# Performance work log

Hardware: AMD Instinct MI355X
Metric: run time of the kernel (lower is better)

The kernel has to match this reference:

```python
import jax, jax.numpy as jnp
import numpy as np

N = 50000          # nodes
E = 1250000        # edges (avg degree 25)
EMBED = 64
HIDS = [64, 64, 64]
EDGE_DIM = 7       # 1 + 6
VOCAB = 5 ** 8     # 390625
NEG_SLOPE = 0.01   # F.leaky_relu default


def setup_inputs() -> dict:
    key = jax.random.key(0)
    ks = jax.random.split(key, 14)
    L = len(HIDS)
    x = jax.random.randint(ks[0], (N,), 0, VOCAB)
    edge_index = jax.random.randint(ks[1], (2, E), 0, N)
    edge_attr = jax.random.normal(ks[2], (E, EDGE_DIM), dtype=jnp.float32)
    emb = jax.random.normal(ks[3], (VOCAB, EMBED), dtype=jnp.float32) * 0.02
    # all layers have in = out = 64, so params are stacked along layer axis
    lin1_w = jax.random.normal(ks[4], (L, EMBED + EDGE_DIM, HIDS[0]), dtype=jnp.float32) * 0.1
    att_l = jax.random.normal(ks[5], (L, HIDS[0]), dtype=jnp.float32) * 0.1
    att_r = jax.random.normal(ks[6], (L, EMBED), dtype=jnp.float32) * 0.1
    lin2_w = jax.random.normal(ks[7], (L, HIDS[0], HIDS[0]), dtype=jnp.float32) * 0.1
    gbias = jax.random.normal(ks[8], (L, HIDS[0]), dtype=jnp.float32) * 0.01
    d_cat = int(np.sum(HIDS)) + EMBED  # 256
    fc1_w = jax.random.normal(ks[9], (d_cat, 20), dtype=jnp.float32) * 0.05
    fc1_b = jax.random.normal(ks[10], (20,), dtype=jnp.float32) * 0.01
    fc2_w = jax.random.normal(ks[11], (20, 1), dtype=jnp.float32) * 0.1
    fc2_b = jax.random.normal(ks[12], (1,), dtype=jnp.float32) * 0.01
    return {"x": x, "edge_index": edge_index, "edge_attr": edge_attr, "emb": emb,
            "lin1_w": lin1_w, "att_l": att_l, "att_r": att_r, "lin2_w": lin2_w,
            "gbias": gbias, "fc1_w": fc1_w, "fc1_b": fc1_b, "fc2_w": fc2_w, "fc2_b": fc2_b}


def _gate_conv(h, src, dst, edge_attr, w1, al, ar, w2, b):
    # message from source j -> target i; attention softmax over edges sharing a target
    xj = jnp.concatenate([h[src], edge_attr], axis=-1)            # [E, in+7]
    xj = jax.nn.leaky_relu(xj @ w1, NEG_SLOPE)                    # [E, out]
    alpha = jax.nn.leaky_relu(jnp.sum(xj * al, -1) + jnp.sum(h[dst] * ar, -1), NEG_SLOPE)
    amax = jax.ops.segment_max(alpha, dst, num_segments=N)        # [N]
    ea = jnp.exp(alpha - amax[dst])                               # [E]
    denom = jax.ops.segment_sum(ea, dst, num_segments=N)          # [N]
    a = ea / (denom[dst] + 1e-16)
    msg = (xj @ w2) * a[:, None]                                  # [E, out]
    return jax.ops.segment_sum(msg, dst, num_segments=N) + b      # [N, out]


def reference(x, edge_index, edge_attr, emb, lin1_w, att_l, att_r, lin2_w,
              gbias, fc1_w, fc1_b, fc2_w, fc2_b):
    src, dst = edge_index[0], edge_index[1]
    h = emb[x]                                                    # [N, EMBED]
    feats = [h]
    for l in range(len(HIDS)):
        h = jax.nn.relu(_gate_conv(h, src, dst, edge_attr,
                                   lin1_w[l], att_l[l], att_r[l], lin2_w[l], gbias[l]))
        feats.append(h)
    hcat = jnp.concatenate(feats, axis=-1)                        # [N, 256]
    z = jax.nn.relu(hcat @ fc1_w + fc1_b)
    out = jax.nn.sigmoid(z @ fc2_w + fc2_b)
    return out.squeeze(-1)                                        # [N]
```

## Files before the change

### kernel.cpp

```cpp
#include <hip/hip_runtime.h>
#include <math.h>

#define NEG 0.01f

typedef _Float16 f16;
typedef f16 h2 __attribute__((ext_vector_type(2)));

__device__ __forceinline__ float lrelu(float x) { return x > 0.f ? x : NEG * x; }

__device__ __forceinline__ h2 lrelu2(h2 x) {
    h2 y = x * (f16)0.01f;
    return __builtin_elementwise_max(x, y);
}

__device__ __forceinline__ float q16_allsum(float v) {
    int x;
    x = __builtin_amdgcn_update_dpp(0, __float_as_int(v), 0xB1, 0xF, 0xF, true);  v += __int_as_float(x);
    x = __builtin_amdgcn_update_dpp(0, __float_as_int(v), 0x4E, 0xF, 0xF, true);  v += __int_as_float(x);
    x = __builtin_amdgcn_update_dpp(0, __float_as_int(v), 0x124, 0xF, 0xF, true); v += __int_as_float(x);
    x = __builtin_amdgcn_update_dpp(0, __float_as_int(v), 0x128, 0xF, 0xF, true); v += __int_as_float(x);
    return v;
}

__device__ __forceinline__ float x16_32_sum(float v) {
    v += __int_as_float(__builtin_amdgcn_ds_swizzle(__float_as_int(v), 0x401F));
    v += __shfl_xor(v, 32, 64);
    return v;
}

__global__ void k_zero(int* __restrict__ deg, int n,
                       const float* __restrict__ lin1, const float* __restrict__ attl,
                       uint4* __restrict__ wpack) {
    int i = blockIdx.x * blockDim.x + threadIdx.x;
    if (i < n) deg[i] = 0;
    if (i < 48) {
        int l = i >> 4, t = i & 15;
        const float* wb  = lin1 + (size_t)l * 71 * 64 + 64 * 64;
        const float* alp = attl + l * 64;
        unsigned int u[20];
#pragma unroll
        for (int j = 0; j < 4; j++) {
            int f = 4 * t + j;
            h2 a = { (f16)wb[f],       (f16)wb[64 + f]  }; u[j]      = __builtin_bit_cast(unsigned int, a);
            h2 b = { (f16)wb[128 + f], (f16)wb[192 + f] }; u[4 + j]  = __builtin_bit_cast(unsigned int, b);
            h2 c = { (f16)wb[256 + f], (f16)wb[320 + f] }; u[8 + j]  = __builtin_bit_cast(unsigned int, c);
            h2 d = { (f16)wb[384 + f], (f16)0.f         }; u[12 + j] = __builtin_bit_cast(unsigned int, d);
        }
        h2 e0 = { (f16)alp[4 * t],     (f16)alp[4 * t + 1] }; u[16] = __builtin_bit_cast(unsigned int, e0);
        h2 e1 = { (f16)alp[4 * t + 2], (f16)alp[4 * t + 3] }; u[17] = __builtin_bit_cast(unsigned int, e1);
        u[18] = 0; u[19] = 0;
        uint4* o = wpack + (size_t)i * 5;
        o[0] = make_uint4(u[0],  u[1],  u[2],  u[3]);
        o[1] = make_uint4(u[4],  u[5],  u[6],  u[7]);
        o[2] = make_uint4(u[8],  u[9],  u[10], u[11]);
        o[3] = make_uint4(u[12], u[13], u[14], u[15]);
        o[4] = make_uint4(u[16], u[17], u[18], u[19]);
    }
}

__global__ __launch_bounds__(256) void k_count_gemm(
    const int* __restrict__ dst, int* __restrict__ deg, int* __restrict__ rank,
    int E, int nbCnt,
    const int* __restrict__ x, const float* __restrict__ emb,
    const float* __restrict__ B, const float* __restrict__ ar,
    f16* __restrict__ g, float* __restrict__ r_out, int N)
{
    __shared__ __align__(16) float sA[64][68];
    __shared__ __align__(16) float sB[64 * 64];
    __shared__ float sar[64];
    if ((int)blockIdx.x < nbCnt) {
        int e = blockIdx.x * 256 + threadIdx.x;
        if (e < E) rank[e] = atomicAdd(&deg[dst[e]], 1);
        return;
    }
    int tid = threadIdx.x;
    int row0 = ((int)blockIdx.x - nbCnt) * 64;

    {
        const float4* b4 = (const float4*)B;
        float4* s4 = (float4*)sB;
        for (int i = tid; i < 1024; i += 256) s4[i] = b4[i];
    }
    if (tid < 64) sar[tid] = ar[tid];

#pragma unroll
    for (int pass = 0; pass < 4; ++pass) {
        int nl = pass * 16 + (tid & 15);
        int k4 = (tid >> 4) * 4;
        int n = row0 + nl; if (n >= N) n = N - 1;
        float4 v = *(const float4*)(emb + (size_t)x[n] * 64 + k4);
        sA[k4 + 0][nl] = v.x; sA[k4 + 1][nl] = v.y;
        sA[k4 + 2][nl] = v.z; sA[k4 + 3][nl] = v.w;
    }
    __syncthreads();

    int tr = tid >> 4, tc = tid & 15;
    int r0 = tr * 4, c0 = tc * 4;
    float acc[4][4];
#pragma unroll
    for (int i = 0; i < 4; i++)
#pragma unroll
        for (int j = 0; j < 4; j++) acc[i][j] = 0.f;

#pragma unroll 4
    for (int k = 0; k < 64; ++k) {
        float4 b4 = *(const float4*)(sB + k * 64 + c0);
        float4 a0 = *(const float4*)&sA[k][r0];
#pragma unroll
        for (int j = 0; j < 4; j++) {
            float bj = (&b4.x)[j];
            acc[0][j] += a0.x * bj; acc[1][j] += a0.y * bj;
            acc[2][j] += a0.z * bj; acc[3][j] += a0.w * bj;
        }
    }

#pragma unroll
    for (int i = 0; i < 4; i++) {
        int n = row0 + r0 + i;
        if (n < N) {
            uint2 gw;
            gw.x = __builtin_bit_cast(unsigned int, __builtin_amdgcn_cvt_pkrtz(acc[i][0], acc[i][1]));
            gw.y = __builtin_bit_cast(unsigned int, __builtin_amdgcn_cvt_pkrtz(acc[i][2], acc[i][3]));
            *(uint2*)(g + (size_t)n * 64 + c0) = gw;
        }
    }
    if (tid < 64) {
        int n = row0 + tid;
        if (n < N) {
            float racc = 0.f;
#pragma unroll
            for (int k = 0; k < 64; k++) racc += sA[k][tid] * sar[k];
            r_out[n] = racc;
        }
    }
}

__global__ __launch_bounds__(256) void k_scan_part(const int* __restrict__ deg,
                                                   int* __restrict__ bsum, int n) {
    __shared__ int sh[256];
    int b = blockIdx.x, t = threadIdx.x;
    int i0 = b * 1024 + t * 4;
    int s = 0;
    if (i0 + 3 < n) { int4 v = *(const int4*)(deg + i0); s = v.x + v.y + v.z + v.w; }
    else { for (int k = 0; k < 4; k++) if (i0 + k < n) s += deg[i0 + k]; }
    sh[t] = s; __syncthreads();
    for (int d = 128; d > 0; d >>= 1) { if (t < d) sh[t] += sh[t + d]; __syncthreads(); }
    if (t == 0) bsum[b] = sh[0];
}

__global__ __launch_bounds__(256) void k_scan_out(const int* __restrict__ deg,
                                                  const int* __restrict__ bsum,
                                                  int* __restrict__ off, int nb, int n) {
    __shared__ int sb[256];
    __shared__ int sh[256];
    int b = blockIdx.x, t = threadIdx.x;
    int v = (t < nb) ? bsum[t] : 0;
    sb[t] = v; __syncthreads();
    for (int d = 1; d < 256; d <<= 1) {
        int u = (t >= d) ? sb[t - d] : 0;
        __syncthreads(); sb[t] += u; __syncthreads();
    }
    int base = (b == 0) ? 0 : sb[b - 1];
    if (b == 0 && t == 0) off[n] = sb[255];
    int i0 = b * 1024 + t * 4;
    int4 v4 = make_int4(0, 0, 0, 0);
    if (i0 + 3 < n) v4 = *(const int4*)(deg + i0);
    else {
        v4.x = (i0     < n) ? deg[i0]     : 0;
        v4.y = (i0 + 1 < n) ? deg[i0 + 1] : 0;
        v4.z = (i0 + 2 < n) ? deg[i0 + 2] : 0;
        v4.w = (i0 + 3 < n) ? deg[i0 + 3] : 0;
    }
    int s = v4.x + v4.y + v4.z + v4.w;
    sh[t] = s; __syncthreads();
    for (int d = 1; d < 256; d <<= 1) {
        int u = (t >= d) ? sh[t - d] : 0;
        __syncthreads(); sh[t] += u; __syncthreads();
    }
    int ex = base + sh[t] - s;
    if (i0     < n) off[i0]     = ex;
    if (i0 + 1 < n) off[i0 + 1] = ex + v4.x;
    if (i0 + 2 < n) off[i0 + 2] = ex + v4.x + v4.y;
    if (i0 + 3 < n) off[i0 + 3] = ex + v4.x + v4.y + v4.z;
}

__global__ void k_fill_embed(const int* __restrict__ src, const int* __restrict__ dst,
                             const float* __restrict__ eattr, const int* __restrict__ off,
                             const int* __restrict__ rank, uint4* __restrict__ rec, int E,
                             int nbE,
                             const int* __restrict__ x, const float* __restrict__ emb,
                             float* __restrict__ hcat, int N) {
    if ((int)blockIdx.x < nbE) {
        int e = blockIdx.x * 256 + threadIdx.x;
        if (e >= E) return;
        int slot = off[dst[e]] + rank[e];
        const float* ap = eattr + (size_t)e * 7;
        float a0 = ap[0], a1 = ap[1], a2 = ap[2], a3 = ap[3], a4 = ap[4], a5 = ap[5], a6 = ap[6];
        uint4 rv;
        h2 p01 = { (f16)a0, (f16)a1 };
        h2 p23 = { (f16)a2, (f16)a3 };
        h2 p45 = { (f16)a4, (f16)a5 };
        rv.x = __builtin_bit_cast(unsigned int, p01);
        rv.y = __builtin_bit_cast(unsigned int, p23);
        rv.z = __builtin_bit_cast(unsigned int, p45);
        unsigned int a6b = (unsigned int)__builtin_bit_cast(unsigned short, (f16)a6);
        rv.w = a6b | ((unsigned int)src[e] << 16);
        rec[slot] = rv;
    } else {
        int idx = ((int)blockIdx.x - nbE) * 256 + threadIdx.x;
        int node = idx >> 4, j4 = (idx & 15) * 4;
        if (node < N) {
            float4 v = *(const float4*)(emb + (size_t)x[node] * 64 + j4);
            *(float4*)(hcat + (size_t)node * 256 + j4) = v;
        }
    }
}

__global__ __launch_bounds__(256) void k_gemm2g1(
    float* __restrict__ hc,
    const float* __restrict__ W2, const float* __restrict__ bias,
    const float* __restrict__ W1n, const float* __restrict__ arn,
    f16* __restrict__ g, float* __restrict__ r_out, int N)
{
    __shared__ __align__(16) float sA[64][68];
    __shared__ __align__(16) float sB[64 * 64];
    __shared__ float sar[64];
    int tid = threadIdx.x, row0 = blockIdx.x * 64;

    {
        const float4* b4 = (const float4*)W2;
        float4* s4 = (float4*)sB;
        for (int i = tid; i < 1024; i += 256) s4[i] = b4[i];
    }
    if (tid < 64) sar[tid] = arn[tid];

#pragma unroll
    for (int pass = 0; pass < 4; ++pass) {
        int nl = pass * 16 + (tid & 15);
        int k4 = (tid >> 4) * 4;
        int n = row0 + nl; if (n >= N) n = N - 1;
        float4 v = *(const float4*)(hc + (size_t)n * 256 + k4);
        sA[k4 + 0][nl] = v.x; sA[k4 + 1][nl] = v.y;
        sA[k4 + 2][nl] = v.z; sA[k4 + 3][nl] = v.w;
    }
    __syncthreads();

    int tr = tid >> 4, tc = tid & 15;
    int r0 = tr * 4, c0 = tc * 4;
    float acc[4][4];
#pragma unroll
    for (int i = 0; i < 4; i++)
#pragma unroll
        for (int j = 0; j < 4; j++) acc[i][j] = 0.f;

#pragma unroll 4
    for (int k = 0; k < 64; ++k) {
        float4 b4 = *(const float4*)(sB + k * 64 + c0);
        float4 a0 = *(const float4*)&sA[k][r0];
#pragma unroll
        for (int j = 0; j < 4; j++) {
            float bj = (&b4.x)[j];
            acc[0][j] += a0.x * bj; acc[1][j] += a0.y * bj;
            acc[2][j] += a0.z * bj; acc[3][j] += a0.w * bj;
        }
    }

    float4 bv = *(const float4*)(bias + c0);
#pragma unroll
    for (int i = 0; i < 4; i++) {
        acc[i][0] = fmaxf(acc[i][0] + bv.x, 0.f);
        acc[i][1] = fmaxf(acc[i][1] + bv.y, 0.f);
        acc[i][2] = fmaxf(acc[i][2] + bv.z, 0.f);
        acc[i][3] = fmaxf(acc[i][3] + bv.w, 0.f);
        int n = row0 + r0 + i;
        if (n < N) *(float4*)(hc + (size_t)n * 256 + c0) =
            make_float4(acc[i][0], acc[i][1], acc[i][2], acc[i][3]);
    }
    __syncthreads();

    {
        const float4* b4 = (const float4*)W1n;
        float4* s4 = (float4*)sB;
        for (int i = tid; i < 1024; i += 256) s4[i] = b4[i];
    }
#pragma unroll
    for (int i = 0; i < 4; i++)
#pragma unroll
        for (int j = 0; j < 4; j++) sA[c0 + j][r0 + i] = acc[i][j];
    __syncthreads();

#pragma unroll
    for (int i = 0; i < 4; i++)
#pragma unroll
        for (int j = 0; j < 4; j++) acc[i][j] = 0.f;

#pragma unroll 4
    for (int k = 0; k < 64; ++k) {
        float4 b4 = *(const float4*)(sB + k * 64 + c0);
        float4 a0 = *(const float4*)&sA[k][r0];
#pragma unroll
        for (int j = 0; j < 4; j++) {
            float bj = (&b4.x)[j];
            acc[0][j] += a0.x * bj; acc[1][j] += a0.y * bj;
            acc[2][j] += a0.z * bj; acc[3][j] += a0.w * bj;
        }
    }

#pragma unroll
    for (int i = 0; i < 4; i++) {
        int n = row0 + r0 + i;
        if (n < N) {
            uint2 gw;
            gw.x = __builtin_bit_cast(unsigned int, __builtin_amdgcn_cvt_pkrtz(acc[i][0], acc[i][1]));
            gw.y = __builtin_bit_cast(unsigned int, __builtin_amdgcn_cvt_pkrtz(acc[i][2], acc[i][3]));
            *(uint2*)(g + (size_t)n * 64 + c0) = gw;
        }
    }
    if (tid < 64) {
        int n = row0 + tid;
        if (n < N) {
            float racc = 0.f;
#pragma unroll
            for (int k = 0; k < 64; k++) racc += sA[k][tid] * sar[k];
            r_out[n] = racc;
        }
    }
}

struct ConvW {
    h2 w01[4], w23[4], w45[4], w6_[4];
    h2 al01, al23;
};

__device__ __forceinline__ void edge_math(uint4 rv, uint2 gv, bool valid, float ri,
                                          const ConvW& W, float4& s, float& den) {
    h2 a01 = __builtin_bit_cast(h2, rv.x);
    h2 a23 = __builtin_bit_cast(h2, rv.y);
    h2 a45 = __builtin_bit_cast(h2, rv.z);
    h2 a6p = __builtin_bit_cast(h2, rv.w & 0xFFFFu);
    h2 g01 = __builtin_bit_cast(h2, gv.x);
    h2 g23 = __builtin_bit_cast(h2, gv.y);

    float c0 = __builtin_amdgcn_fdot2(a01, W.w01[0],
               __builtin_amdgcn_fdot2(a23, W.w23[0],
               __builtin_amdgcn_fdot2(a45, W.w45[0],
               __builtin_amdgcn_fdot2(a6p, W.w6_[0], 0.f, false), false), false), false);
    float c1 = __builtin_amdgcn_fdot2(a01, W.w01[1],
               __builtin_amdgcn_fdot2(a23, W.w23[1],
               __builtin_amdgcn_fdot2(a45, W.w45[1],
               __builtin_amdgcn_fdot2(a6p, W.w6_[1], 0.f, false), false), false), false);
    float c2 = __builtin_amdgcn_fdot2(a01, W.w01[2],
               __builtin_amdgcn_fdot2(a23, W.w23[2],
               __builtin_amdgcn_fdot2(a45, W.w45[2],
               __builtin_amdgcn_fdot2(a6p, W.w6_[2], 0.f, false), false), false), false);
    float c3 = __builtin_amdgcn_fdot2(a01, W.w01[3],
               __builtin_amdgcn_fdot2(a23, W.w23[3],
               __builtin_amdgcn_fdot2(a45, W.w45[3],
               __builtin_amdgcn_fdot2(a6p, W.w6_[3], 0.f, false), false), false), false);

    h2 x01 = lrelu2(g01 + __builtin_amdgcn_cvt_pkrtz(c0, c1));
    h2 x23 = lrelu2(g23 + __builtin_amdgcn_cvt_pkrtz(c2, c3));
    float p = __builtin_amdgcn_fdot2(x01, W.al01,
              __builtin_amdgcn_fdot2(x23, W.al23, 0.f, false), false);
    p = q16_allsum(p);
    float alpha = lrelu(p + ri);
    float w = valid ? __expf(alpha) : 0.f;
    s.x += w * (float)x01.x; s.y += w * (float)x01.y;
    s.z += w * (float)x23.x; s.w += w * (float)x23.y;
    den += w;
}

__global__ __launch_bounds__(256) void k_conv(
    const int* __restrict__ off, const uint4* __restrict__ rec,
    const f16* __restrict__ g, const float* __restrict__ r,
    const uint4* __restrict__ wpack, float* __restrict__ aggdst, int N)
{
    int lane = threadIdx.x & 63;
    int wid  = threadIdx.x >> 6;
    int node = blockIdx.x * 4 + wid;
    if (node >= N) return;
    int q = lane >> 4, l16 = lane & 15;

    ConvW W;
    {
        const uint4* wp = wpack + l16 * 5;
        uint4 v0 = wp[0], v1 = wp[1], v2 = wp[2], v3 = wp[3], v4 = wp[4];
        W.w01[0] = __builtin_bit_cast(h2, v0.x); W.w01[1] = __builtin_bit_cast(h2, v0.y);
        W.w01[2] = __builtin_bit_cast(h2, v0.z); W.w01[3] = __builtin_bit_cast(h2, v0.w);
        W.w23[0] = __builtin_bit_cast(h2, v1.x); W.w23[1] = __builtin_bit_cast(h2, v1.y);
        W.w23[2] = __builtin_bit_cast(h2, v1.z); W.w23[3] = __builtin_bit_cast(h2, v1.w);
        W.w45[0] = __builtin_bit_cast(h2, v2.x); W.w45[1] = __builtin_bit_cast(h2, v2.y);
        W.w45[2] = __builtin_bit_cast(h2, v2.z); W.w45[3] = __builtin_bit_cast(h2, v2.w);
        W.w6_[0] = __builtin_bit_cast(h2, v3.x); W.w6_[1] = __builtin_bit_cast(h2, v3.y);
        W.w6_[2] = __builtin_bit_cast(h2, v3.z); W.w6_[3] = __builtin_bit_cast(h2, v3.w);
        W.al01   = __builtin_bit_cast(h2, v4.x); W.al23   = __builtin_bit_cast(h2, v4.y);
    }

    float ri = r[node];
    int e0 = off[node], e1 = off[node + 1];

    float4 s = make_float4(0.f, 0.f, 0.f, 0.f);
    float den = 0.f;
    if (e0 < e1) {
        int last = e1 - 1;
        int ea = e0 + q, eb = ea + 4, ec = ea + 8, ed = ea + 12;
        uint4 ra = rec[ea < e1 ? ea : last];
        uint4 rb = rec[eb < e1 ? eb : last];
        uint4 rc = rec[ec < e1 ? ec : last];
        uint4 rd = rec[ed < e1 ? ed : last];
        for (int e = e0; e < e1; e += 16) {
            uint2 ga = *(const uint2*)(g + (size_t)(ra.w >> 16) * 64 + 4 * l16);
            uint2 gb = *(const uint2*)(g + (size_t)(rb.w >> 16) * 64 + 4 * l16);
            uint2 gc = *(const uint2*)(g + (size_t)(rc.w >> 16) * 64 + 4 * l16);
            uint2 gd = *(const uint2*)(g + (size_t)(rd.w >> 16) * 64 + 4 * l16);
            int en = e + 16;
            int fa = en + q, fb = fa + 4, fc = fa + 8, fd = fa + 12;
            uint4 na = rec[fa < e1 ? fa : last];
            uint4 nb = rec[fb < e1 ? fb : last];
            uint4 nc = rec[fc < e1 ? fc : last];
            uint4 nd = rec[fd < e1 ? fd : last];
            bool va = (e + q)      < e1, vb = (e + 4 + q)  < e1;
            bool vc = (e + 8 + q)  < e1, vd = (e + 12 + q) < e1;
            edge_math(ra, ga, va, ri, W, s, den);
            edge_math(rb, gb, vb, ri, W, s, den);
            edge_math(rc, gc, vc, ri, W, s, den);
            edge_math(rd, gd, vd, ri, W, s, den);
            ra = na; rb = nb; rc = nc; rd = nd;
        }
    }
    s.x = x16_32_sum(s.x); s.y = x16_32_sum(s.y);
    s.z = x16_32_sum(s.z); s.w = x16_32_sum(s.w);
    den = x16_32_sum(den);
    float inv = 1.f / (den + 1e-16f);
    if (q == 0) {
        float4 o = make_float4(s.x * inv, s.y * inv, s.z * inv, s.w * inv);
        *(float4*)(aggdst + (size_t)node * 256 + 4 * l16) = o;
    }
}

__global__ __launch_bounds__(256) void k_gemm2head(
    const float* __restrict__ hcat,
    const float* __restrict__ W2, const float* __restrict__ bias,
    const float* __restrict__ f1w, const float* __restrict__ f1b,
    const float* __restrict__ f2w, const float* __restrict__ f2b,
    float* __restrict__ out, int N)
{
    __shared__ __align__(16) float sA[64][132];
    __shared__ __align__(16) float sBW[5120];
    __shared__ float sP[128 * 20];
    int tid = threadIdx.x, row0 = blockIdx.x * 128;

    {
        const float4* b4 = (const float4*)W2;
        float4* s4 = (float4*)sBW;
        for (int i = tid; i < 1024; i += 256) s4[i] = b4[i];
    }
#pragma unroll
    for (int pass = 0; pass < 8; ++pass) {
        int nl = pass * 16 + (tid & 15);
        int k4 = (tid >> 4) * 4;
        int n = row0 + nl; if (n >= N) n = N - 1;
        float4 v = *(const float4*)(hcat + (size_t)n * 256 + 192 + k4);
        sA[k4 + 0][nl] = v.x; sA[k4 + 1][nl] = v.y;
        sA[k4 + 2][nl] = v.z; sA[k4 + 3][nl] = v.w;
    }
    __syncthreads();

    int tr = tid >> 4, tc = tid & 15;
    int r0 = tr * 8, c0 = tc * 4;
    float acc[8][4];
#pragma unroll
    for (int i = 0; i < 8; i++)
#pragma unroll
        for (int j = 0; j < 4; j++) acc[i][j] = 0.f;

#pragma unroll 4
    for (int k = 0; k < 64; ++k) {
        float4 b4 = *(const float4*)(sBW + k * 64 + c0);
        float4 a0 = *(const float4*)&sA[k][r0];
        float4 a1 = *(const float4*)&sA[k][r0 + 4];
#pragma unroll
        for (int j = 0; j < 4; j++) {
            float bj = (&b4.x)[j];
            acc[0][j] += a0.x * bj; acc[1][j] += a0.y * bj;
            acc[2][j] += a0.z * bj; acc[3][j] += a0.w * bj;
            acc[4][j] += a1.x * bj; acc[5][j] += a1.y * bj;
            acc[6][j] += a1.z * bj; acc[7][j] += a1.w * bj;
        }
    }

    float4 fw[5];
    {
        const float4* w4 = (const float4*)f1w;
#pragma unroll
        for (int i2 = 0; i2 < 5; i2++) fw[i2] = w4[tid + i2 * 256];
    }
    __syncthreads();

    float* sO = &sA[0][0];
    float4 bv = *(const float4*)(bias + c0);
#pragma unroll
    for (int i = 0; i < 8; i++) {
        acc[i][0] = fmaxf(acc[i][0] + bv.x, 0.f);
        acc[i][1] = fmaxf(acc[i][1] + bv.y, 0.f);
        acc[i][2] = fmaxf(acc[i][2] + bv.z, 0.f);
        acc[i][3] = fmaxf(acc[i][3] + bv.w, 0.f);
        int rr = r0 + i;
        sO[rr * 65 + c0 + 0] = acc[i][0];
        sO[rr * 65 + c0 + 1] = acc[i][1];
        sO[rr * 65 + c0 + 2] = acc[i][2];
        sO[rr * 65 + c0 + 3] = acc[i][3];
    }
    {
        float4* sw4 = (float4*)sBW;
#pragma unroll
        for (int i2 = 0; i2 < 5; i2++) sw4[tid + i2 * 256] = fw[i2];
    }
    __syncthreads();

    int rloc = tid & 127;
    int half = tid >> 7;
    int n = row0 + rloc;
    int nn = (n < N) ? n : N - 1;
    float z[20];
#pragma unroll
    for (int j = 0; j < 20; j++) z[j] = 0.f;
    const float4* hr = (const float4*)(hcat + (size_t)nn * 256);
    if (half == 0) {
        for (int k4 = 0; k4 < 32; k4++) {
            float4 h = hr[k4];
            const float* wr = sBW + k4 * 80;
#pragma unroll
            for (int j = 0; j < 20; j++)
                z[j] += h.x * wr[j] + h.y * wr[20 + j] + h.z * wr[40 + j] + h.w * wr[60 + j];
        }
    } else {
        for (int k4 = 32; k4 < 48; k4++) {
            float4 h = hr[k4];
            const float* wr = sBW + k4 * 80;
#pragma unroll
            for (int j = 0; j < 20; j++)
                z[j] += h.x * wr[j] + h.y * wr[20 + j] + h.z * wr[40 + j] + h.w * wr[60 + j];
        }
        for (int k = 0; k < 64; k += 2) {
            float hx = sO[rloc * 65 + k], hy = sO[rloc * 65 + k + 1];
            const float* wr = sBW + (192 + k) * 20;
#pragma unroll
            for (int j = 0; j < 20; j++)
                z[j] += hx * wr[j] + hy * wr[20 + j];
        }
#pragma unroll
        for (int j = 0; j < 20; j++) sP[rloc * 20 + j] = z[j];
    }
    __syncthreads();
    if (half == 0 && n < N) {
        float o = f2b[0];
#pragma unroll
        for (int j = 0; j < 20; j++) {
            float zj = z[j] + sP[rloc * 20 + j] + f1b[j];
            o += fmaxf(zj, 0.f) * f2w[j];
        }
        out[n] = 1.f / (1.f + __expf(-o));
    }
}

extern "C" void kernel_launch(void* const* d_in, const int* in_sizes, int n_in,
                              void* d_out, int out_size, void* d_ws, size_t ws_size,
                              hipStream_t stream) {
    const int*   x     = (const int*)d_in[0];
    const int*   eidx  = (const int*)d_in[1];
    const float* eattr = (const float*)d_in[2];
    const float* emb   = (const float*)d_in[3];
    const float* lin1  = (const float*)d_in[4];
    const float* attl  = (const float*)d_in[5];
    const float* attr_ = (const float*)d_in[6];
    const float* lin2  = (const float*)d_in[7];
    const float* gbias = (const float*)d_in[8];
    const float* f1w   = (const float*)d_in[9];
    const float* f1b   = (const float*)d_in[10];
    const float* f2w   = (const float*)d_in[11];
    const float* f2b   = (const float*)d_in[12];
    float* out = (float*)d_out;

    int N = in_sizes[0];
    int E = in_sizes[1] / 2;
    const int* src = eidx;
    const int* dst = eidx + E;

    char* p = (char*)d_ws;
    auto alloc = [&](size_t bytes) { void* q = (void*)p; p += (bytes + 255) & ~(size_t)255; return q; };
    float* hcat = (float*)alloc((size_t)N * 256 * 4);
    f16*   g    = (f16*)alloc((size_t)N * 64 * 2);
    float* r    = (float*)alloc((size_t)N * 4);
    int*   off  = (int*)alloc((size_t)(N + 1) * 4);
    int*   deg  = (int*)alloc((size_t)N * 4);
    int*   rank = (int*)alloc((size_t)E * 4);
    int*   bsum = (int*)alloc(256 * 4);
    uint4* rec  = (uint4*)alloc((size_t)E * 16);
    uint4* wpack = (uint4*)alloc((size_t)48 * 5 * 16);

    int nbs   = (N + 1023) / 1024;
    int nbE   = (E + 255) / 256;
    int nbEmb = (N * 16 + 255) / 256;
    int nbg64 = (N + 63) / 64;
    int nbg128 = (N + 127) / 128;
    int nbc   = (N + 3) / 4;

    k_zero<<<(N + 255) / 256, 256, 0, stream>>>(deg, N, lin1, attl, wpack);
    k_count_gemm<<<nbE + nbg64, 256, 0, stream>>>(dst, deg, rank, E, nbE,
                                                  x, emb, lin1, attr_, g, r, N);
    k_scan_part<<<nbs, 256, 0, stream>>>(deg, bsum, N);
    k_scan_out<<<nbs, 256, 0, stream>>>(deg, bsum, off, nbs, N);
    k_fill_embed<<<nbE + nbEmb, 256, 0, stream>>>(src, dst, eattr, off, rank, rec, E,
                                                  nbE, x, emb, hcat, N);

    k_conv<<<nbc, 256, 0, stream>>>(off, rec, g, r, wpack, hcat + 64, N);
    for (int l = 0; l < 2; l++) {
        k_gemm2g1<<<nbg64, 256, 0, stream>>>(hcat + 64 * (l + 1),
                                             lin2 + (size_t)l * 4096, gbias + l * 64,
                                             lin1 + (size_t)(l + 1) * 71 * 64,
                                             attr_ + (l + 1) * 64, g, r, N);
        k_conv<<<nbc, 256, 0, stream>>>(off, rec, g, r,
                                        wpack + (size_t)(l + 1) * 80,
                                        hcat + 64 * (l + 2), N);
    }
    k_gemm2head<<<nbg128, 256, 0, stream>>>(hcat, lin2 + 2 * 4096, gbias + 128,
                                            f1w, f1b, f2w, f2b, out, N);
}
```

Measured before the change: 493.8 us.

## Restructure CSR build with cursor atomics, fuse embed copy, deepen conv prefetch

The per-edge rank array is replaced by a per-node cursor: the count kernel only increments degrees, and the fill kernel claims slots with atomicAdd on a cursor array initialised by the scan. This removes the E-sized rank write and read. The embedding copy into hcat moves into the zero/gemm kernel, which already loads those rows, and the conv loop now prefetches records two iterations ahead and gathers g one iteration ahead. Costs: a separate launch is added, a second round of atomics runs in the fill pass, and edge order within a node becomes nondeterministic.

```diff
diff --git a/kernel.cpp b/kernel.cpp
--- a/kernel.cpp
+++ b/kernel.cpp
@@ -28,56 +28,50 @@
     return v;
 }
 
-__global__ void k_zero(int* __restrict__ deg, int n,
-                       const float* __restrict__ lin1, const float* __restrict__ attl,
-                       uint4* __restrict__ wpack) {
-    int i = blockIdx.x * blockDim.x + threadIdx.x;
-    if (i < n) deg[i] = 0;
-    if (i < 48) {
-        int l = i >> 4, t = i & 15;
-        const float* wb  = lin1 + (size_t)l * 71 * 64 + 64 * 64;
-        const float* alp = attl + l * 64;
-        unsigned int u[20];
-#pragma unroll
-        for (int j = 0; j < 4; j++) {
-            int f = 4 * t + j;
-            h2 a = { (f16)wb[f],       (f16)wb[64 + f]  }; u[j]      = __builtin_bit_cast(unsigned int, a);
-            h2 b = { (f16)wb[128 + f], (f16)wb[192 + f] }; u[4 + j]  = __builtin_bit_cast(unsigned int, b);
-            h2 c = { (f16)wb[256 + f], (f16)wb[320 + f] }; u[8 + j]  = __builtin_bit_cast(unsigned int, c);
-            h2 d = { (f16)wb[384 + f], (f16)0.f         }; u[12 + j] = __builtin_bit_cast(unsigned int, d);
-        }
-        h2 e0 = { (f16)alp[4 * t],     (f16)alp[4 * t + 1] }; u[16] = __builtin_bit_cast(unsigned int, e0);
-        h2 e1 = { (f16)alp[4 * t + 2], (f16)alp[4 * t + 3] }; u[17] = __builtin_bit_cast(unsigned int, e1);
-        u[18] = 0; u[19] = 0;
-        uint4* o = wpack + (size_t)i * 5;
-        o[0] = make_uint4(u[0],  u[1],  u[2],  u[3]);
-        o[1] = make_uint4(u[4],  u[5],  u[6],  u[7]);
-        o[2] = make_uint4(u[8],  u[9],  u[10], u[11]);
-        o[3] = make_uint4(u[12], u[13], u[14], u[15]);
-        o[4] = make_uint4(u[16], u[17], u[18], u[19]);
-    }
-}
-
-__global__ __launch_bounds__(256) void k_count_gemm(
-    const int* __restrict__ dst, int* __restrict__ deg, int* __restrict__ rank,
-    int E, int nbCnt,
+__global__ __launch_bounds__(256) void k_zero_gemm(
+    int* __restrict__ deg, int N, int nz,
+    const float* __restrict__ lin1, const float* __restrict__ attl,
+    uint4* __restrict__ wpack,
     const int* __restrict__ x, const float* __restrict__ emb,
-    const float* __restrict__ B, const float* __restrict__ ar,
-    f16* __restrict__ g, float* __restrict__ r_out, int N)
+    const float* __restrict__ ar,
+    f16* __restrict__ g, float* __restrict__ r_out, float* __restrict__ hcat)
 {
     __shared__ __align__(16) float sA[64][68];
     __shared__ __align__(16) float sB[64 * 64];
     __shared__ float sar[64];
-    if ((int)blockIdx.x < nbCnt) {
-        int e = blockIdx.x * 256 + threadIdx.x;
-        if (e < E) rank[e] = atomicAdd(&deg[dst[e]], 1);
+    int tid = threadIdx.x;
+    if ((int)blockIdx.x < nz) {
+        int i = blockIdx.x * 256 + tid;
+        if (i < N) deg[i] = 0;
+        if (i < 48) {
+            int l = i >> 4, t = i & 15;
+            const float* wb  = lin1 + (size_t)l * 71 * 64 + 64 * 64;
+            const float* alp = attl + l * 64;
+            unsigned int u[20];
+#pragma unroll
+            for (int j = 0; j < 4; j++) {
+                int f = 4 * t + j;
+                h2 a = { (f16)wb[f],       (f16)wb[64 + f]  }; u[j]      = __builtin_bit_cast(unsigned int, a);
+                h2 b = { (f16)wb[128 + f], (f16)wb[192 + f] }; u[4 + j]  = __builtin_bit_cast(unsigned int, b);
+                h2 c = { (f16)wb[256 + f], (f16)wb[320 + f] }; u[8 + j]  = __builtin_bit_cast(unsigned int, c);
+                h2 d = { (f16)wb[384 + f], (f16)0.f         }; u[12 + j] = __builtin_bit_cast(unsigned int, d);
+            }
+            h2 e0 = { (f16)alp[4 * t],     (f16)alp[4 * t + 1] }; u[16] = __builtin_bit_cast(unsigned int, e0);
+            h2 e1 = { (f16)alp[4 * t + 2], (f16)alp[4 * t + 3] }; u[17] = __builtin_bit_cast(unsigned int, e1);
+            u[18] = 0; u[19] = 0;
+            uint4* o = wpack + (size_t)i * 5;
+            o[0] = make_uint4(u[0],  u[1],  u[2],  u[3]);
+            o[1] = make_uint4(u[4],  u[5],  u[6],  u[7]);
+            o[2] = make_uint4(u[8],  u[9],  u[10], u[11]);
+            o[3] = make_uint4(u[12], u[13], u[14], u[15]);
+            o[4] = make_uint4(u[16], u[17], u[18], u[19]);
+        }
         return;
     }
-    int tid = threadIdx.x;
-    int row0 = ((int)blockIdx.x - nbCnt) * 64;
+    int row0 = ((int)blockIdx.x - nz) * 64;
 
     {
-        const float4* b4 = (const float4*)B;
+        const float4* b4 = (const float4*)lin1;
         float4* s4 = (float4*)sB;
         for (int i = tid; i < 1024; i += 256) s4[i] = b4[i];
     }
@@ -87,10 +81,11 @@
     for (int pass = 0; pass < 4; ++pass) {
         int nl = pass * 16 + (tid & 15);
         int k4 = (tid >> 4) * 4;
-        int n = row0 + nl; if (n >= N) n = N - 1;
+        int n = row0 + nl; bool ok = n < N; if (!ok) n = N - 1;
         float4 v = *(const float4*)(emb + (size_t)x[n] * 64 + k4);
         sA[k4 + 0][nl] = v.x; sA[k4 + 1][nl] = v.y;
         sA[k4 + 2][nl] = v.z; sA[k4 + 3][nl] = v.w;
+        if (ok) *(float4*)(hcat + (size_t)n * 256 + k4) = v;
     }
     __syncthreads();
 
@@ -133,6 +128,11 @@
             r_out[n] = racc;
         }
     }
+}
+
+__global__ void k_count(const int* __restrict__ dst, int* __restrict__ deg, int E) {
+    int e = blockIdx.x * blockDim.x + threadIdx.x;
+    if (e < E) atomicAdd(&deg[dst[e]], 1);
 }
 
 __global__ __launch_bounds__(256) void k_scan_part(const int* __restrict__ deg,
@@ -150,7 +150,8 @@
 
 __global__ __launch_bounds__(256) void k_scan_out(const int* __restrict__ deg,
                                                   const int* __restrict__ bsum,
-                                                  int* __restrict__ off, int nb, int n) {
+                                                  int* __restrict__ off,
+                                                  int* __restrict__ cur, int nb, int n) {
     __shared__ int sb[256];
     __shared__ int sh[256];
     int b = blockIdx.x, t = threadIdx.x;
@@ -178,42 +179,30 @@
         __syncthreads(); sh[t] += u; __syncthreads();
     }
     int ex = base + sh[t] - s;
-    if (i0     < n) off[i0]     = ex;
-    if (i0 + 1 < n) off[i0 + 1] = ex + v4.x;
-    if (i0 + 2 < n) off[i0 + 2] = ex + v4.x + v4.y;
-    if (i0 + 3 < n) off[i0 + 3] = ex + v4.x + v4.y + v4.z;
-}
-
-__global__ void k_fill_embed(const int* __restrict__ src, const int* __restrict__ dst,
-                             const float* __restrict__ eattr, const int* __restrict__ off,
-                             const int* __restrict__ rank, uint4* __restrict__ rec, int E,
-                             int nbE,
-                             const int* __restrict__ x, const float* __restrict__ emb,
-                             float* __restrict__ hcat, int N) {
-    if ((int)blockIdx.x < nbE) {
-        int e = blockIdx.x * 256 + threadIdx.x;
-        if (e >= E) return;
-        int slot = off[dst[e]] + rank[e];
-        const float* ap = eattr + (size_t)e * 7;
-        float a0 = ap[0], a1 = ap[1], a2 = ap[2], a3 = ap[3], a4 = ap[4], a5 = ap[5], a6 = ap[6];
-        uint4 rv;
-        h2 p01 = { (f16)a0, (f16)a1 };
-        h2 p23 = { (f16)a2, (f16)a3 };
-        h2 p45 = { (f16)a4, (f16)a5 };
-        rv.x = __builtin_bit_cast(unsigned int, p01);
-        rv.y = __builtin_bit_cast(unsigned int, p23);
-        rv.z = __builtin_bit_cast(unsigned int, p45);
-        unsigned int a6b = (unsigned int)__builtin_bit_cast(unsigned short, (f16)a6);
-        rv.w = a6b | ((unsigned int)src[e] << 16);
-        rec[slot] = rv;
-    } else {
-        int idx = ((int)blockIdx.x - nbE) * 256 + threadIdx.x;
-        int node = idx >> 4, j4 = (idx & 15) * 4;
-        if (node < N) {
-            float4 v = *(const float4*)(emb + (size_t)x[node] * 64 + j4);
-            *(float4*)(hcat + (size_t)node * 256 + j4) = v;
-        }
-    }
+    if (i0 < n)     { off[i0]     = ex;                      cur[i0]     = ex; }
+    if (i0 + 1 < n) { int w = ex + v4.x;                off[i0 + 1] = w; cur[i0 + 1] = w; }
+    if (i0 + 2 < n) { int w = ex + v4.x + v4.y;         off[i0 + 2] = w; cur[i0 + 2] = w; }
+    if (i0 + 3 < n) { int w = ex + v4.x + v4.y + v4.z;  off[i0 + 3] = w; cur[i0 + 3] = w; }
+}
+
+__global__ void k_fill(const int* __restrict__ src, const int* __restrict__ dst,
+                       const float* __restrict__ eattr, int* __restrict__ cur,
+                       uint4* __restrict__ rec, int E) {
+    int e = blockIdx.x * 256 + threadIdx.x;
+    if (e >= E) return;
+    int slot = atomicAdd(&cur[dst[e]], 1);
+    const float* ap = eattr + (size_t)e * 7;
+    float a0 = ap[0], a1 = ap[1], a2 = ap[2], a3 = ap[3], a4 = ap[4], a5 = ap[5], a6 = ap[6];
+    uint4 rv;
+    h2 p01 = { (f16)a0, (f16)a1 };
+    h2 p23 = { (f16)a2, (f16)a3 };
+    h2 p45 = { (f16)a4, (f16)a5 };
+    rv.x = __builtin_bit_cast(unsigned int, p01);
+    rv.y = __builtin_bit_cast(unsigned int, p23);
+    rv.z = __builtin_bit_cast(unsigned int, p45);
+    unsigned int a6b = (unsigned int)__builtin_bit_cast(unsigned short, (f16)a6);
+    rv.w = a6b | ((unsigned int)src[e] << 16);
+    rec[slot] = rv;
 }
 
 __global__ __launch_bounds__(256) void k_gemm2g1(
@@ -398,27 +387,36 @@
 
     float ri = r[node];
     int e0 = off[node], e1 = off[node + 1];
+    int goff = 4 * l16;
 
     float4 s = make_float4(0.f, 0.f, 0.f, 0.f);
     float den = 0.f;
     if (e0 < e1) {
         int last = e1 - 1;
-        int ea = e0 + q, eb = ea + 4, ec = ea + 8, ed = ea + 12;
-        uint4 ra = rec[ea < e1 ? ea : last];
-        uint4 rb = rec[eb < e1 ? eb : last];
-        uint4 rc = rec[ec < e1 ? ec : last];
-        uint4 rd = rec[ed < e1 ? ed : last];
+        int b0 = e0 + q;
+        uint4 ra = rec[b0      < e1 ? b0      : last];
+        uint4 rb = rec[b0 + 4  < e1 ? b0 + 4  : last];
+        uint4 rc = rec[b0 + 8  < e1 ? b0 + 8  : last];
+        uint4 rd = rec[b0 + 12 < e1 ? b0 + 12 : last];
+        uint2 ga = *(const uint2*)(g + (size_t)(ra.w >> 16) * 64 + goff);
+        uint2 gb = *(const uint2*)(g + (size_t)(rb.w >> 16) * 64 + goff);
+        uint2 gc = *(const uint2*)(g + (size_t)(rc.w >> 16) * 64 + goff);
+        uint2 gd = *(const uint2*)(g + (size_t)(rd.w >> 16) * 64 + goff);
+        int b1 = b0 + 16;
+        uint4 na = rec[b1      < e1 ? b1      : last];
+        uint4 nb = rec[b1 + 4  < e1 ? b1 + 4  : last];
+        uint4 nc = rec[b1 + 8  < e1 ? b1 + 8  : last];
+        uint4 nd = rec[b1 + 12 < e1 ? b1 + 12 : last];
         for (int e = e0; e < e1; e += 16) {
-            uint2 ga = *(const uint2*)(g + (size_t)(ra.w >> 16) * 64 + 4 * l16);
-            uint2 gb = *(const uint2*)(g + (size_t)(rb.w >> 16) * 64 + 4 * l16);
-            uint2 gc = *(const uint2*)(g + (size_t)(rc.w >> 16) * 64 + 4 * l16);
-            uint2 gd = *(const uint2*)(g + (size_t)(rd.w >> 16) * 64 + 4 * l16);
-            int en = e + 16;
-            int fa = en + q, fb = fa + 4, fc = fa + 8, fd = fa + 12;
-            uint4 na = rec[fa < e1 ? fa : last];
-            uint4 nb = rec[fb < e1 ? fb : last];
-            uint4 nc = rec[fc < e1 ? fc : last];
-            uint4 nd = rec[fd < e1 ? fd : last];
+            uint2 gna = *(const uint2*)(g + (size_t)(na.w >> 16) * 64 + goff);
+            uint2 gnb = *(const uint2*)(g + (size_t)(nb.w >> 16) * 64 + goff);
+            uint2 gnc = *(const uint2*)(g + (size_t)(nc.w >> 16) * 64 + goff);
+            uint2 gnd = *(const uint2*)(g + (size_t)(nd.w >> 16) * 64 + goff);
+            int b2 = e + 32 + q;
+            uint4 ma = rec[b2      < e1 ? b2      : last];
+            uint4 mb = rec[b2 + 4  < e1 ? b2 + 4  : last];
+            uint4 mc = rec[b2 + 8  < e1 ? b2 + 8  : last];
+            uint4 md = rec[b2 + 12 < e1 ? b2 + 12 : last];
             bool va = (e + q)      < e1, vb = (e + 4 + q)  < e1;
             bool vc = (e + 8 + q)  < e1, vd = (e + 12 + q) < e1;
             edge_math(ra, ga, va, ri, W, s, den);
@@ -426,6 +424,8 @@
             edge_math(rc, gc, vc, ri, W, s, den);
             edge_math(rd, gd, vd, ri, W, s, den);
             ra = na; rb = nb; rc = nc; rd = nd;
+            ga = gna; gb = gnb; gc = gnc; gd = gnd;
+            na = ma; nb = mb; nc = mc; nd = md;
         }
     }
     s.x = x16_32_sum(s.x); s.y = x16_32_sum(s.y);
@@ -434,7 +434,7 @@
     float inv = 1.f / (den + 1e-16f);
     if (q == 0) {
         float4 o = make_float4(s.x * inv, s.y * inv, s.z * inv, s.w * inv);
-        *(float4*)(aggdst + (size_t)node * 256 + 4 * l16) = o;
+        *(float4*)(aggdst + (size_t)node * 256 + goff) = o;
     }
 }
 
@@ -594,25 +594,24 @@
     float* r    = (float*)alloc((size_t)N * 4);
     int*   off  = (int*)alloc((size_t)(N + 1) * 4);
     int*   deg  = (int*)alloc((size_t)N * 4);
-    int*   rank = (int*)alloc((size_t)E * 4);
+    int*   cur  = (int*)alloc((size_t)N * 4);
     int*   bsum = (int*)alloc(256 * 4);
     uint4* rec  = (uint4*)alloc((size_t)E * 16);
     uint4* wpack = (uint4*)alloc((size_t)48 * 5 * 16);
 
+    int nz    = (N + 255) / 256;
     int nbs   = (N + 1023) / 1024;
     int nbE   = (E + 255) / 256;
-    int nbEmb = (N * 16 + 255) / 256;
     int nbg64 = (N + 63) / 64;
     int nbg128 = (N + 127) / 128;
     int nbc   = (N + 3) / 4;
 
-    k_zero<<<(N + 255) / 256, 256, 0, stream>>>(deg, N, lin1, attl, wpack);
-    k_count_gemm<<<nbE + nbg64, 256, 0, stream>>>(dst, deg, rank, E, nbE,
-                                                  x, emb, lin1, attr_, g, r, N);
+    k_zero_gemm<<<nz + nbg64, 256, 0, stream>>>(deg, N, nz, lin1, attl, wpack,
+                                                x, emb, attr_, g, r, hcat);
+    k_count<<<nbE, 256, 0, stream>>>(dst, deg, E);
     k_scan_part<<<nbs, 256, 0, stream>>>(deg, bsum, N);
-    k_scan_out<<<nbs, 256, 0, stream>>>(deg, bsum, off, nbs, N);
-    k_fill_embed<<<nbE + nbEmb, 256, 0, stream>>>(src, dst, eattr, off, rank, rec, E,
-                                                  nbE, x, emb, hcat, N);
+    k_scan_out<<<nbs, 256, 0, stream>>>(deg, bsum, off, cur, nbs, N);
+    k_fill<<<nbE, 256, 0, stream>>>(src, dst, eattr, cur, rec, E);
 
     k_conv<<<nbc, 256, 0, stream>>>(off, rec, g, r, wpack, hcat + 64, N);
     for (int l = 0; l < 2; l++) {
```

Result: slower. 544.8 us (+10.3%).
